# Kernel tuning notes

Measured on AMD Instinct MI355X. Metric: run time of the kernel, lower is better.

## Reference

```python
import jax, jax.numpy as jnp
import numpy as np

A = 9
C = 80
TOPK = 1000            # topk_candidates
NMS_THRESH = 0.5
SCORE_THRESH = 0.05
DET_PER_IMG = 100      # detections_per_img
BBOX_XFORM_CLIP = float(np.log(1000.0 / 16.0))
CLASS_OFFSET = 4096.0  # > any clipped coordinate -> class-aware NMS trick


def setup_inputs() -> dict:
    key = jax.random.key(0)
    ks = jax.random.split(key, 4)
    B = 8
    levels = [(128, 128, 4096, 8), (64, 64, 2048, 16), (32, 32, 1024, 32)]  # H, W, K, stride
    inp = {}
    for i, (H, W, K, stride) in enumerate(levels):
        k1, k2, k3, k4, k5, k6, k7, k8 = jax.random.split(ks[i], 8)
        # plausible anchor boxes (x1, y1, x2, y2) with positive width/height
        cx = jax.random.uniform(k1, (B, H, W, A)) * (W * stride)
        cy = jax.random.uniform(k2, (B, H, W, A)) * (H * stride)
        w = 16.0 + jax.random.uniform(k3, (B, H, W, A)) * 112.0
        h = 16.0 + jax.random.uniform(k4, (B, H, W, A)) * 112.0
        anch = jnp.stack([cx - 0.5 * w, cy - 0.5 * h, cx + 0.5 * w, cy + 0.5 * h], axis=-1)
        # [B, H, W, A, 4] -> [B, 4A, H, W] (A groups of 4 along channel, matching permute(1,2,0) + reshape(-1,4))
        inp[f"anchors_{i}"] = jnp.transpose(anch.reshape(B, H, W, 4 * A), (0, 3, 1, 2)).astype(jnp.float32)
        coords = jnp.stack(
            [jax.random.randint(k5, (B, K), 0, H), jax.random.randint(k6, (B, K), 0, W)], axis=-1
        ).astype(jnp.int32)
        inp[f"coords_{i}"] = coords
        inp[f"score_logits_{i}"] = (jax.random.normal(k7, (B, K, A * C)) * 2.0 - 2.0).astype(jnp.float32)
        inp[f"regs_{i}"] = (jax.random.normal(k8, (B, K, A * 4)) * 0.2).astype(jnp.float32)
    inp["image_shapes"] = jnp.full((B, 2), 1024.0, dtype=jnp.float32)  # (h, w) per image
    return inp


def _decode(boxes, deltas, img_hw):
    # boxes, deltas: [N, 4] (x1, y1, x2, y2) / (dx, dy, dw, dh)
    x1, y1, x2, y2 = boxes[:, 0], boxes[:, 1], boxes[:, 2], boxes[:, 3]
    w = x2 - x1
    h = y2 - y1
    cx = x1 + 0.5 * w
    cy = y1 + 0.5 * h
    dx, dy = deltas[:, 0], deltas[:, 1]
    dw = jnp.minimum(deltas[:, 2], BBOX_XFORM_CLIP)
    dh = jnp.minimum(deltas[:, 3], BBOX_XFORM_CLIP)
    pcx = dx * w + cx
    pcy = dy * h + cy
    pw = jnp.exp(dw) * w
    ph = jnp.exp(dh) * h
    ih, iw = img_hw[0], img_hw[1]
    nx1 = jnp.clip(pcx - 0.5 * pw, 0.0, iw)
    ny1 = jnp.clip(pcy - 0.5 * ph, 0.0, ih)
    nx2 = jnp.clip(pcx + 0.5 * pw, 0.0, iw)
    ny2 = jnp.clip(pcy + 0.5 * ph, 0.0, ih)
    return jnp.stack([nx1, ny1, nx2, ny2], axis=-1)


def _level(anchor_map, coords, logits, regs, img_hw):
    # anchor_map: [4A, H, W]; coords: [K, 2]; logits: [K, A*C]; regs: [K, A*4]
    bb = jnp.transpose(anchor_map, (1, 2, 0))[coords[:, 0], coords[:, 1]]  # [K, 4A]
    boxes = bb.reshape(-1, 4)            # [K*A, 4]
    deltas = regs.reshape(-1, 4)         # [K*A, 4]
    dec = _decode(boxes, deltas, img_hw)
    scores = jax.nn.sigmoid(logits.reshape(-1, C))  # [K*A, C]
    flat = scores.reshape(-1)                       # [K*A*C]
    k = min(TOPK, flat.shape[0])
    top_s, idx = jax.lax.top_k(flat, k)
    return dec[idx // C], top_s, (idx % C)


def _pairwise_iou(b):
    area = (b[:, 2] - b[:, 0]) * (b[:, 3] - b[:, 1])
    lt = jnp.maximum(b[:, None, :2], b[None, :, :2])
    rb = jnp.minimum(b[:, None, 2:], b[None, :, 2:])
    wh = jnp.clip(rb - lt, 0.0)
    inter = wh[..., 0] * wh[..., 1]
    return inter / (area[:, None] + area[None, :] - inter + 1e-9)


def _nms(boxes, scores, labels):
    # class-aware NMS with fixed-size output [DET_PER_IMG, 6]
    order = jnp.argsort(-scores)
    b = boxes[order]
    s = scores[order]
    l = labels[order]
    iou = _pairwise_iou(b + l.astype(b.dtype)[:, None] * CLASS_OFFSET)  # [N, N]
    N = s.shape[0]
    idxs = jnp.arange(N)
    valid = s > SCORE_THRESH

    def body(i, keep):
        sup = (iou[i] > NMS_THRESH) & (idxs > i) & keep[i]
        return keep & ~sup

    keep = jax.lax.fori_loop(0, N, body, valid)
    masked = jnp.where(keep, s, -1.0)
    top_s, top_i = jax.lax.top_k(masked, DET_PER_IMG)
    pad = top_s > 0.0
    out_b = jnp.where(pad[:, None], b[top_i], 0.0)
    out_l = jnp.where(pad, l[top_i], -1).astype(b.dtype)
    return jnp.concatenate([out_b, top_s[:, None], out_l[:, None]], axis=-1)  # [DET, 6]


def _per_image(a0, a1, a2, c0, c1, c2, s0, s1, s2, r0, r1, r2, hw):
    parts = [
        _level(a, c, sl, r, hw)
        for a, c, sl, r in zip((a0, a1, a2), (c0, c1, c2), (s0, s1, s2), (r0, r1, r2))
    ]
    boxes = jnp.concatenate([p[0] for p in parts], axis=0)
    scores = jnp.concatenate([p[1] for p in parts], axis=0)
    labels = jnp.concatenate([p[2] for p in parts], axis=0)
    return _nms(boxes, scores, labels)


def reference(anchors_0, anchors_1, anchors_2, coords_0, coords_1, coords_2,
              score_logits_0, score_logits_1, score_logits_2,
              regs_0, regs_1, regs_2, image_shapes):
    # returns [B, DET_PER_IMG, 6] = (x1, y1, x2, y2, score, label); padded rows have score -1, label -1
    return jax.vmap(_per_image)(
        anchors_0, anchors_1, anchors_2,
        coords_0, coords_1, coords_2,
        score_logits_0, score_logits_1, score_logits_2,
        regs_0, regs_1, regs_2, image_shapes,
    )
```

## Files before the change

### kernel.cpp

```cpp
#include <hip/hip_runtime.h>

typedef unsigned long long u64;
typedef unsigned int u32;

#define NIMG 8
#define NLVL 3
#define TOPKN 1000
#define NC3 3000
#define DETS 100
#define PRETH 3.0f
#define NBINS 3072
#define LCAP 2048
#define MROWS 256
#define MLDS 128
#define NW 47
#define NWP 48
#define NSUB 64
#define SUBCAP 768
#define GPAD 16
#define BG 8
#define MB 64

#define NBLK0 2880
#define NBLK1 1440
#define NBLK2 720
#define NBLKTOT 5040

__device__ __forceinline__ u32 fmap(float f) {
  u32 b = __float_as_uint(f);
  return (b & 0x80000000u) ? ~b : (b | 0x80000000u);
}
__device__ __forceinline__ float funmap(u32 u) {
  u32 b = (u & 0x80000000u) ? (u & 0x7FFFFFFFu) : ~u;
  return __uint_as_float(b);
}

__global__ __launch_bounds__(256) void k_prefilter(
    const float* __restrict__ lg0, const float* __restrict__ lg1,
    const float* __restrict__ lg2, u64* __restrict__ dense,
    u32* __restrict__ gcnt) {
  const int tid = threadIdx.x, wave = tid >> 6, lane = tid & 63;
  int blk = blockIdx.x;
  const float* lg; int imgElems, lblk, lvl;
  if (blk < NBLK0)              { lg = lg0; imgElems = 2949120; lblk = blk; lvl = 0; }
  else if (blk < NBLK0 + NBLK1) { lg = lg1; imgElems = 1474560; lblk = blk - NBLK0; lvl = 1; }
  else                          { lg = lg2; imgElems = 737280;  lblk = blk - NBLK0 - NBLK1; lvl = 2; }
  int ce = lblk * 8192 + wave * 2048;
  int img = ce / imgElems;
  int flatBase = ce - img * imgElems;
  const float* src = lg + (size_t)img * imgElems;
  const int dst = img * NLVL + lvl;
  const int sub = (lblk * 4 + wave) & (NSUB - 1);
  u64 lmask = (1ull << lane) - 1ull;
  float va[32];
#pragma unroll
  for (int r = 0; r < 8; ++r) {
    const float4 v = *(const float4*)(src + flatBase + r * 256 + lane * 4);
    va[r * 4 + 0] = v.x; va[r * 4 + 1] = v.y;
    va[r * 4 + 2] = v.z; va[r * 4 + 3] = v.w;
  }
  __builtin_amdgcn_sched_barrier(0);
  int total = 0;
#pragma unroll
  for (int u = 0; u < 32; ++u) total += __popcll(__ballot(va[u] > PRETH));
  u32 base = 0;
  if (lane == 0 && total)
    base = atomicAdd(&gcnt[(dst * NSUB + sub) * GPAD], (u32)total);
  base = (u32)__shfl((int)base, 0);
  u64* db = dense + ((size_t)dst * NSUB + sub) * SUBCAP;
  int off = 0;
#pragma unroll
  for (int u = 0; u < 32; ++u) {
    bool p = va[u] > PRETH;
    u64 m = __ballot(p);
    if (p) {
      int idx = flatBase + (u >> 2) * 256 + lane * 4 + (u & 3);
      u32 pos = base + (u32)(off + __popcll(m & lmask));
      if (pos < SUBCAP) db[pos] = ((u64)fmap(va[u]) << 32) | (u64)(~(u32)idx);
    }
    off += __popcll(m);
  }
}

__global__ __launch_bounds__(1024) void k_select(
    const u64* __restrict__ dense, const u32* __restrict__ gcnt,
    u64* __restrict__ topk) {
  __shared__ u32 hist[NBINS];
  __shared__ u64 lk[LCAP];
  __shared__ u32 wsum[16], wpre[16];
  __shared__ u32 scnt[NSUB];
  __shared__ int sT, sM;
  const int bi = blockIdx.x;
  const int tid = threadIdx.x, wave = tid >> 6, lane = tid & 63;

  const u64 SAFE = ((u64)0x3E5FFFFFu << 32) | 0xFFFFFFFFull;
  if (tid < TOPKN) topk[(size_t)bi * TOPKN + tid] = SAFE;
  for (int i = tid; i < NBINS; i += 1024) hist[i] = 0;
  if (tid < NSUB) {
    u32 c = gcnt[(bi * NSUB + tid) * GPAD];
    scnt[tid] = c > SUBCAP ? SUBCAP : c;
  }
  if (tid == 0) { sM = 0; sT = 0; }
  __syncthreads();

  const u64* src = dense + (size_t)bi * NSUB * SUBCAP;
  for (int s = wave; s < NSUB; s += 16) {
    u32 c = scnt[s];
    const u64* sp = src + (size_t)s * SUBCAP;
    for (u32 i = lane; i < c; i += 64) {
      u32 bin = ((u32)(sp[i] >> 32) - 0xC0000000u) >> 13;
      if (bin > NBINS - 1) bin = NBINS - 1;
      atomicAdd(&hist[bin], 1u);
    }
  }
  __syncthreads();

  const int h0 = NBINS - 1 - tid * 3;
  u32 a0 = hist[h0], a1 = hist[h0 - 1], a2 = hist[h0 - 2];
  u32 s = a0 + a1 + a2;
  u32 inc = s;
#pragma unroll
  for (int d = 1; d < 64; d <<= 1) {
    u32 t = (u32)__shfl_up((int)inc, d);
    if (lane >= d) inc += t;
  }
  if (lane == 63) wsum[wave] = inc;
  __syncthreads();
  if (tid < 16) {
    u32 w = wsum[tid];
    u32 wi = w;
#pragma unroll
    for (int d = 1; d < 16; d <<= 1) {
      u32 t = (u32)__shfl_up((int)wi, d);
      if (tid >= d) wi += t;
    }
    wpre[tid] = wi - w;
  }
  __syncthreads();
  u32 excl = wpre[wave] + (inc - s);
  if (excl < TOPKN && excl + s >= TOPKN) {
    u32 acc = excl + a0;
    int T;
    if (acc >= TOPKN) T = h0;
    else { acc += a1; T = (acc >= TOPKN) ? h0 - 1 : h0 - 2; }
    sT = T;
  }
  __syncthreads();
  const int T = sT;

  for (int s2 = wave; s2 < NSUB; s2 += 16) {
    u32 c = scnt[s2];
    const u64* sp = src + (size_t)s2 * SUBCAP;
    for (u32 i = lane; i < c; i += 64) {
      u64 key = sp[i];
      u32 bin = ((u32)(key >> 32) - 0xC0000000u) >> 13;
      if (bin > NBINS - 1) bin = NBINS - 1;
      if ((int)bin >= T) {
        int q = atomicAdd(&sM, 1);
        if (q < LCAP) lk[q] = key;
      }
    }
  }
  __syncthreads();
  int M = sM; if (M > LCAP) M = LCAP;
  u64 k0 = 0, k1 = 0;
  const bool have0 = tid < M, have1 = tid + 1024 < M;
  if (have0) k0 = lk[tid];
  if (have1) k1 = lk[tid + 1024];
  int r0 = 0, r1 = 0;
  for (int j = 0; j < M; ++j) {
    u64 kj = lk[j];
    r0 += (kj > k0);
    r1 += (kj > k1);
  }
  if (have0 && r0 < TOPKN) topk[(size_t)bi * TOPKN + r0] = k0;
  if (have1 && r1 < TOPKN) topk[(size_t)bi * TOPKN + r1] = k1;
}

__global__ __launch_bounds__(512) void k_build(
    const u64* __restrict__ topk,
    const float* __restrict__ an0, const float* __restrict__ an1, const float* __restrict__ an2,
    const int* __restrict__ co0, const int* __restrict__ co1, const int* __restrict__ co2,
    const float* __restrict__ rg0, const float* __restrict__ rg1, const float* __restrict__ rg2,
    const float* __restrict__ ishape,
    float4* __restrict__ sbox, float* __restrict__ sscore, int* __restrict__ slabel) {
  __shared__ u64 keys[NC3];
  const int bb = blockIdx.x, b = bb >> 3, g = bb & (BG - 1);
  const int tid = threadIdx.x;
  const double ih = (double)ishape[b * 2 + 0];
  const double iw = (double)ishape[b * 2 + 1];
  const double CLIPV = 4.1351665567423563;
  for (int c = tid; c < NC3; c += 512) {
    int l = c / 1000, pos = c - l * 1000;
    u64 key = topk[(size_t)(b * NLVL + l) * TOPKN + pos];
    keys[c] = (key & 0xFFFFFFFF00000000ull) | (u64)(~(u32)c);
  }
  __syncthreads();
  if (tid < 375) {
    int c = g * 375 + tid;
    int l = c / 1000, pos = c - l * 1000;
    u64 key = topk[(size_t)(b * NLVL + l) * TOPKN + pos];
    u32 hi = (u32)(key >> 32);
    u32 flat = ~((u32)key);
    float logit = funmap(hi);
    int cls = (int)(flat % 80u);
    int bidx = (int)(flat / 80u);
    int k = bidx / 9, a = bidx - k * 9;
    const float* an; const int* co; const float* rg; int K, H, W;
    if (l == 0)      { an = an0; co = co0; rg = rg0; K = 4096; H = 128; W = 128; }
    else if (l == 1) { an = an1; co = co1; rg = rg1; K = 2048; H = 64;  W = 64;  }
    else             { an = an2; co = co2; rg = rg2; K = 1024; H = 32;  W = 32;  }
    if (k >= K) k = K - 1;
    int y = co[(b * K + k) * 2 + 0], x = co[(b * K + k) * 2 + 1];
    int HW = H * W;
    const float* ap = an + (size_t)(b * 36 + a * 4) * HW + y * W + x;
    double x1 = (double)ap[0], y1 = (double)ap[HW];
    double x2 = (double)ap[2 * HW], y2 = (double)ap[3 * HW];
    const float* rp = rg + (size_t)(b * K + k) * 36 + a * 4;
    double dx = (double)rp[0], dy = (double)rp[1];
    double dw = fmin((double)rp[2], CLIPV), dh = fmin((double)rp[3], CLIPV);
    double w = x2 - x1, h = y2 - y1;
    double cx = x1 + 0.5 * w, cy = y1 + 0.5 * h;
    double pcx = dx * w + cx, pcy = dy * h + cy;
    double pw = exp(dw) * w, ph = exp(dh) * h;
    double nx1 = fmin(fmax(pcx - 0.5 * pw, 0.0), iw);
    double ny1 = fmin(fmax(pcy - 0.5 * ph, 0.0), ih);
    double nx2 = fmin(fmax(pcx + 0.5 * pw, 0.0), iw);
    double ny2 = fmin(fmax(pcy + 0.5 * ph, 0.0), ih);
    float4 mb = make_float4((float)nx1, (float)ny1, (float)nx2, (float)ny2);
    float ms = (float)(1.0 / (1.0 + exp(-(double)logit)));
    u64 mykey = keys[c];
    int rank = pos;
#pragma unroll
    for (int m = 0; m < 3; ++m) {
      if (m == l) continue;
      int lo = 0, hi2 = 1000, base = m * 1000;
      while (lo < hi2) {
        int mid = (lo + hi2) >> 1;
        if (keys[base + mid] > mykey) lo = mid + 1; else hi2 = mid;
      }
      rank += lo;
    }
    sbox[(size_t)b * NC3 + rank] = mb;
    sscore[(size_t)b * NC3 + rank] = ms;
    slabel[(size_t)b * NC3 + rank] = cls;
  }
}

__global__ __launch_bounds__(256) void k_mask(
    const float4* __restrict__ sbox, const int* __restrict__ slabel,
    u64* __restrict__ mask) {
  __shared__ float4 qb[NC3];
  __shared__ float ar[NC3];
  const int img = blockIdx.x >> 6;
  const int r0 = (blockIdx.x & 63) * 4;
  const int tid = threadIdx.x, wave = tid >> 6, lane = tid & 63;
  for (int i = tid; i < NC3; i += 256) {
    float4 bx = sbox[(size_t)img * NC3 + i];
    float off = (float)slabel[(size_t)img * NC3 + i] * 4096.0f;
    float4 q = make_float4(bx.x + off, bx.y + off, bx.z + off, bx.w + off);
    qb[i] = q;
    ar[i] = (q.z - q.x) * (q.w - q.y);
  }
  __syncthreads();
  u64* mbase = mask + (size_t)img * MROWS * NWP;
#pragma unroll
  for (int q = 0; q < 4; ++q) {
    int i = r0 + q;
    float4 bi = qb[i];
    float ai = ar[i];
    for (int w = wave; w < NW; w += 4) {
      int j = w * 64 + lane;
      bool pred = false;
      if (j > i && j < NC3) {
        float4 bj = qb[j];
        float ltx = fmaxf(bi.x, bj.x), lty = fmaxf(bi.y, bj.y);
        float rbx = fminf(bi.z, bj.z), rby = fminf(bi.w, bj.w);
        float wx = fmaxf(rbx - ltx, 0.f), wy = fmaxf(rby - lty, 0.f);
        float inter = wx * wy;
        float denom = ((ai + ar[j]) - inter) + 1e-9f;
        pred = (inter / denom) > 0.5f;
      }
      u64 m = __ballot(pred);
      if (lane == 0) mbase[(size_t)i * NWP + w] = m;
    }
  }
}

__global__ __launch_bounds__(256) void k_serial(
    const float4* __restrict__ sbox, const float* __restrict__ sscore,
    const int* __restrict__ slabel, const u64* __restrict__ mask,
    float* __restrict__ out) {
  __shared__ u64 sm_mask[MLDS * NWP];
  __shared__ float sm_sc[NC3];
  __shared__ int keptIdx[DETS];
  __shared__ int s_cnt;
  const int img = blockIdx.x, tid = threadIdx.x, wave = tid >> 6, lane = tid & 63;
  const u64* mbase = mask + (size_t)img * MROWS * NWP;
  const float* sc = sscore + (size_t)img * NC3;
  for (int i = tid; i < MLDS * NWP; i += 256) sm_mask[i] = mbase[i];
  for (int i = tid; i < NC3; i += 256) sm_sc[i] = sc[i];
  __syncthreads();
  if (wave == 0) {
    u64 mykeep = 0;
    for (int w = 0; w < NW; ++w) {
      int j = w * 64 + lane;
      float s = (j < NC3) ? sm_sc[j] : -1.f;
      u64 m = __ballot(s > 0.05f);
      if (lane == w) mykeep = m;
    }
    u64 pend[4];
    for (int d = 0; d < 4; ++d)
      pend[d] = (lane < NW) ? sm_mask[d * NWP + lane] : 0ull;
    int cnt = 0;
    for (int i = 0; i < NC3; ++i) {
      u64 row = pend[i & 3];
      int nxt = i + 4;
      if (nxt < MROWS)
        pend[i & 3] = (lane < NW)
            ? ((nxt < MLDS) ? sm_mask[nxt * NWP + lane]
                            : mbase[(size_t)nxt * NWP + lane])
            : 0ull;
      int w = i >> 6;
      u64 kw = __shfl(mykeep, w);
      if ((kw >> (i & 63)) & 1ull) {
        if (lane == 0) keptIdx[cnt] = i;
        cnt++;
        if (cnt == DETS) break;
        if (i < MROWS) {
          mykeep &= ~row;
        } else {
          float4 bx = sbox[(size_t)img * NC3 + i];
          float off = (float)slabel[(size_t)img * NC3 + i] * 4096.0f;
          float bix = bx.x + off, biy = bx.y + off;
          float biz = bx.z + off, biw = bx.w + off;
          float ai = (biz - bix) * (biw - biy);
          for (int w2 = 0; w2 < NW; ++w2) {
            int j = w2 * 64 + lane;
            bool pred = false;
            if (j > i && j < NC3) {
              float4 bj = sbox[(size_t)img * NC3 + j];
              float o2 = (float)slabel[(size_t)img * NC3 + j] * 4096.0f;
              float jx = bj.x + o2, jy = bj.y + o2;
              float jz = bj.z + o2, jw = bj.w + o2;
              float aj = (jz - jx) * (jw - jy);
              float ltx = fmaxf(bix, jx), lty = fmaxf(biy, jy);
              float rbx = fminf(biz, jz), rby = fminf(biw, jw);
              float wx = fmaxf(rbx - ltx, 0.f), wy = fmaxf(rby - lty, 0.f);
              float inter = wx * wy;
              float denom = ((ai + aj) - inter) + 1e-9f;
              pred = (inter / denom) > 0.5f;
            }
            u64 m = __ballot(pred);
            if (lane == w2) mykeep &= ~m;
          }
        }
      }
    }
    if (lane == 0) s_cnt = cnt;
  }
  __syncthreads();
  const int cnt = s_cnt;
  for (int s = tid; s < DETS; s += 256) {
    float* o = out + ((size_t)img * DETS + s) * 6;
    if (s < cnt) {
      int i = keptIdx[s];
      float4 bx = sbox[(size_t)img * NC3 + i];
      o[0] = bx.x; o[1] = bx.y; o[2] = bx.z; o[3] = bx.w;
      o[4] = sm_sc[i];
      o[5] = (float)slabel[(size_t)img * NC3 + i];
    } else {
      o[0] = 0.f; o[1] = 0.f; o[2] = 0.f; o[3] = 0.f;
      o[4] = -1.0f; o[5] = -1.0f;
    }
  }
}

extern "C" void kernel_launch(void* const* d_in, const int* in_sizes, int n_in,
                              void* d_out, int out_size, void* d_ws, size_t ws_size,
                              hipStream_t stream) {
  int ia0, ic0, is0, ir0, ia1, ic1, is1, ir1, ia2, ic2, is2, ir2, ihw;
  if (in_sizes[1] == 8 * 4096 * 2) {
    ia0 = 0; ic0 = 1; is0 = 2; ir0 = 3;
    ia1 = 4; ic1 = 5; is1 = 6; ir1 = 7;
    ia2 = 8; ic2 = 9; is2 = 10; ir2 = 11; ihw = 12;
  } else {
    ia0 = 0; ia1 = 1; ia2 = 2;
    ic0 = 3; ic1 = 4; ic2 = 5;
    is0 = 6; is1 = 7; is2 = 8;
    ir0 = 9; ir1 = 10; ir2 = 11; ihw = 12;
  }

  u32* gcnt = (u32*)d_ws;
  u64* dense = (u64*)((char*)d_ws + 98304);
  u64* topk = dense + (size_t)NIMG * NLVL * NSUB * SUBCAP;
  float4* sboxp = (float4*)(topk + NIMG * NLVL * TOPKN);
  float* sscore = (float*)(sboxp + NIMG * NC3);
  int* slabel = (int*)(sscore + NIMG * NC3);
  u64* maskp = (u64*)(slabel + NIMG * NC3);
  float* out = (float*)d_out;

  hipMemsetAsync(d_ws, 0, 98304, stream);

  k_prefilter<<<NBLKTOT, 256, 0, stream>>>(
      (const float*)d_in[is0], (const float*)d_in[is1], (const float*)d_in[is2],
      dense, gcnt);
  k_select<<<NIMG * NLVL, 1024, 0, stream>>>(dense, gcnt, topk);
  k_build<<<NIMG * BG, 512, 0, stream>>>(topk,
      (const float*)d_in[ia0], (const float*)d_in[ia1], (const float*)d_in[ia2],
      (const int*)d_in[ic0], (const int*)d_in[ic1], (const int*)d_in[ic2],
      (const float*)d_in[ir0], (const float*)d_in[ir1], (const float*)d_in[ir2],
      (const float*)d_in[ihw],
      sboxp, sscore, slabel);
  k_mask<<<NIMG * MB, 256, 0, stream>>>(sboxp, slabel, maskp);
  k_serial<<<NIMG, 256, 0, stream>>>(sboxp, sscore, slabel, maskp, out);
}
```

Measured before the change: 338.0 us.

## Halve prefilter work per block, use lane prefix-scan compaction, batch select loads

The prefilter kernel now processes 1024 elements per wave instead of 2048 and doubles the block count. It replaces per-element ballot compaction with a per-lane count followed by a wave prefix scan, so each lane writes its survivors contiguously. In the select kernel, the histogram and candidate-gather loops issue four independent sub-bucket loads together rather than walking sub-buckets one after another, to expose more memory-level parallelism. In exchange, the doubled grid means more atomics on the global counters, and per-lane contiguous writes are less coalesced.

```diff
diff --git a/kernel.cpp b/kernel.cpp
--- a/kernel.cpp
+++ b/kernel.cpp
@@ -21,10 +21,10 @@
 #define BG 8
 #define MB 64
 
-#define NBLK0 2880
-#define NBLK1 1440
-#define NBLK2 720
-#define NBLKTOT 5040
+#define NBLK0 5760
+#define NBLK1 2880
+#define NBLK2 1440
+#define NBLKTOT 10080
 
 __device__ __forceinline__ u32 fmap(float f) {
   u32 b = __float_as_uint(f);
@@ -45,40 +45,44 @@
   if (blk < NBLK0)              { lg = lg0; imgElems = 2949120; lblk = blk; lvl = 0; }
   else if (blk < NBLK0 + NBLK1) { lg = lg1; imgElems = 1474560; lblk = blk - NBLK0; lvl = 1; }
   else                          { lg = lg2; imgElems = 737280;  lblk = blk - NBLK0 - NBLK1; lvl = 2; }
-  int ce = lblk * 8192 + wave * 2048;
+  int ce = lblk * 4096 + wave * 1024;
   int img = ce / imgElems;
   int flatBase = ce - img * imgElems;
   const float* src = lg + (size_t)img * imgElems;
   const int dst = img * NLVL + lvl;
   const int sub = (lblk * 4 + wave) & (NSUB - 1);
-  u64 lmask = (1ull << lane) - 1ull;
-  float va[32];
-#pragma unroll
-  for (int r = 0; r < 8; ++r) {
+  float va[16];
+#pragma unroll
+  for (int r = 0; r < 4; ++r) {
     const float4 v = *(const float4*)(src + flatBase + r * 256 + lane * 4);
     va[r * 4 + 0] = v.x; va[r * 4 + 1] = v.y;
     va[r * 4 + 2] = v.z; va[r * 4 + 3] = v.w;
   }
   __builtin_amdgcn_sched_barrier(0);
-  int total = 0;
-#pragma unroll
-  for (int u = 0; u < 32; ++u) total += __popcll(__ballot(va[u] > PRETH));
+  int myc = 0;
+#pragma unroll
+  for (int u = 0; u < 16; ++u) myc += (va[u] > PRETH) ? 1 : 0;
+  int inc = myc;
+#pragma unroll
+  for (int d = 1; d < 64; d <<= 1) {
+    int t = __shfl_up(inc, d);
+    if (lane >= d) inc += t;
+  }
+  int total = __shfl(inc, 63);
+  int mybase = inc - myc;
   u32 base = 0;
-  if (lane == 0 && total)
+  if (lane == 63 && total)
     base = atomicAdd(&gcnt[(dst * NSUB + sub) * GPAD], (u32)total);
-  base = (u32)__shfl((int)base, 0);
+  base = (u32)__shfl((int)base, 63);
   u64* db = dense + ((size_t)dst * NSUB + sub) * SUBCAP;
-  int off = 0;
-#pragma unroll
-  for (int u = 0; u < 32; ++u) {
-    bool p = va[u] > PRETH;
-    u64 m = __ballot(p);
-    if (p) {
+  u32 pos = base + (u32)mybase;
+#pragma unroll
+  for (int u = 0; u < 16; ++u) {
+    if (va[u] > PRETH) {
       int idx = flatBase + (u >> 2) * 256 + lane * 4 + (u & 3);
-      u32 pos = base + (u32)(off + __popcll(m & lmask));
       if (pos < SUBCAP) db[pos] = ((u64)fmap(va[u]) << 32) | (u64)(~(u32)idx);
-    }
-    off += __popcll(m);
+      pos++;
+    }
   }
 }
 
@@ -104,13 +108,27 @@
   __syncthreads();
 
   const u64* src = dense + (size_t)bi * NSUB * SUBCAP;
-  for (int s = wave; s < NSUB; s += 16) {
-    u32 c = scnt[s];
-    const u64* sp = src + (size_t)s * SUBCAP;
-    for (u32 i = lane; i < c; i += 64) {
-      u32 bin = ((u32)(sp[i] >> 32) - 0xC0000000u) >> 13;
-      if (bin > NBINS - 1) bin = NBINS - 1;
-      atomicAdd(&hist[bin], 1u);
+  const u64* pp[4]; u32 cc[4]; u32 maxc = 0;
+#pragma unroll
+  for (int j = 0; j < 4; ++j) {
+    int s = wave + j * 16;
+    cc[j] = scnt[s];
+    pp[j] = src + (size_t)s * SUBCAP;
+    if (cc[j] > maxc) maxc = cc[j];
+  }
+  for (u32 i = lane; i < maxc; i += 64) {
+    u64 k0 = (i < cc[0]) ? pp[0][i] : 0ull;
+    u64 k1 = (i < cc[1]) ? pp[1][i] : 0ull;
+    u64 k2 = (i < cc[2]) ? pp[2][i] : 0ull;
+    u64 k3 = (i < cc[3]) ? pp[3][i] : 0ull;
+#pragma unroll
+    for (int j = 0; j < 4; ++j) {
+      u64 kk = (j == 0) ? k0 : (j == 1) ? k1 : (j == 2) ? k2 : k3;
+      if (i < cc[j]) {
+        u32 bin = ((u32)(kk >> 32) - 0xC0000000u) >> 13;
+        if (bin > NBINS - 1) bin = NBINS - 1;
+        atomicAdd(&hist[bin], 1u);
+      }
     }
   }
   __syncthreads();
@@ -148,16 +166,21 @@
   __syncthreads();
   const int T = sT;
 
-  for (int s2 = wave; s2 < NSUB; s2 += 16) {
-    u32 c = scnt[s2];
-    const u64* sp = src + (size_t)s2 * SUBCAP;
-    for (u32 i = lane; i < c; i += 64) {
-      u64 key = sp[i];
-      u32 bin = ((u32)(key >> 32) - 0xC0000000u) >> 13;
-      if (bin > NBINS - 1) bin = NBINS - 1;
-      if ((int)bin >= T) {
-        int q = atomicAdd(&sM, 1);
-        if (q < LCAP) lk[q] = key;
+  for (u32 i = lane; i < maxc; i += 64) {
+    u64 k0 = (i < cc[0]) ? pp[0][i] : 0ull;
+    u64 k1 = (i < cc[1]) ? pp[1][i] : 0ull;
+    u64 k2 = (i < cc[2]) ? pp[2][i] : 0ull;
+    u64 k3 = (i < cc[3]) ? pp[3][i] : 0ull;
+#pragma unroll
+    for (int j = 0; j < 4; ++j) {
+      u64 kk = (j == 0) ? k0 : (j == 1) ? k1 : (j == 2) ? k2 : k3;
+      if (i < cc[j]) {
+        u32 bin = ((u32)(kk >> 32) - 0xC0000000u) >> 13;
+        if (bin > NBINS - 1) bin = NBINS - 1;
+        if ((int)bin >= T) {
+          int q = atomicAdd(&sM, 1);
+          if (q < LCAP) lk[q] = kk;
+        }
       }
     }
   }
```

Result: no change. 332.7 us (-1.6%).
